# Kernel tuning notes

Measured on AMD Instinct MI355X. Metric: run time of the kernel, lower is better.

The kernel has to match this reference:

```python
import jax, jax.numpy as jnp
import numpy as np

B, T, E = 4, 2048, 256
H = 8
HD = E // H
FE = 4
L = 4
EPS = 1e-5


def _layernorm(x, g, b):
    mu = jnp.mean(x, axis=-1, keepdims=True)
    var = jnp.mean((x - mu) ** 2, axis=-1, keepdims=True)
    return (x - mu) * jax.lax.rsqrt(var + EPS) * g + b


def setup_inputs() -> dict:
    key = jax.random.key(0)
    ks = jax.random.split(key, 14)
    s = 0.02
    inp = {
        "x": jax.random.normal(ks[0], (B, T, E), dtype=jnp.float32),
        "qkv_w": jax.random.normal(ks[1], (L, E, 3 * E), dtype=jnp.float32) * s,
        "qkv_b": jnp.zeros((L, 3 * E), jnp.float32),
        "out_w": jax.random.normal(ks[2], (L, E, E), dtype=jnp.float32) * s,
        "out_b": jnp.zeros((L, E), jnp.float32),
        "ff1_w": jax.random.normal(ks[3], (L, E, FE * E), dtype=jnp.float32) * s,
        "ff1_b": jnp.zeros((L, FE * E), jnp.float32),
        "ff2_w": jax.random.normal(ks[4], (L, FE * E, E), dtype=jnp.float32) * s,
        "ff2_b": jnp.zeros((L, E), jnp.float32),
        "ln1_g": jnp.ones((L, E), jnp.float32),
        "ln1_b": jnp.zeros((L, E), jnp.float32),
        "ln2_g": jnp.ones((L, E), jnp.float32),
        "ln2_b": jnp.zeros((L, E), jnp.float32),
    }
    return inp


def _fourier_pe(x):
    # freqs over even indices: 10000^(-i/E), i = 0,2,...,E-2  -> E/2 freqs
    freqs = jnp.power(10000.0, -jnp.arange(0, E, 2, dtype=jnp.float32) / E)
    pos = jnp.arange(T, dtype=jnp.float32)[:, None]          # (T,1)
    sinusoid = pos * freqs[None, :]                            # (T, E/2)
    pe = jnp.concatenate([jnp.sin(sinusoid), jnp.cos(sinusoid)], axis=-1)  # (T,E)
    return x + pe[None, :, :]


def _forward(x, qkv_w, qkv_b, out_w, out_b, ff1_w, ff1_b, ff2_w, ff2_b,
             ln1_g, ln1_b, ln2_g, ln2_b):
    x = _fourier_pe(x)
    scale = 1.0 / np.sqrt(HD)
    for i in range(L):
        # attention (dropout = identity at eval)
        qkv = x @ qkv_w[i] + qkv_b[i]                          # (B,T,3E)
        qkv = qkv.reshape(B, T, H, 3, HD)                      # chunk of 3*hd -> (3,hd)
        q, k, v = qkv[..., 0, :], qkv[..., 1, :], qkv[..., 2, :]  # (B,T,H,HD)
        scores = jnp.einsum("bqhd,bkhd->bhqk", q, k) * scale   # (B,H,T,T)
        w = jax.nn.softmax(scores, axis=-1)
        attn = jnp.einsum("bhqk,bkhd->bqhd", w, v).reshape(B, T, E)
        attn = attn @ out_w[i] + out_b[i]
        x = _layernorm(x + attn, ln1_g[i], ln1_b[i])
        # feedforward
        h = jax.nn.relu(x @ ff1_w[i] + ff1_b[i])
        ff = h @ ff2_w[i] + ff2_b[i]
        x = _layernorm(x + ff, ln2_g[i], ln2_b[i])
    return x


def reference(x, qkv_w, qkv_b, out_w, out_b, ff1_w, ff1_b, ff2_w, ff2_b,
              ln1_g, ln1_b, ln2_g, ln2_b):
    return _forward(x, qkv_w, qkv_b, out_w, out_b, ff1_w, ff1_b, ff2_w, ff2_b,
                    ln1_g, ln1_b, ln2_g, ln2_b)
```

## Files before the change

kernel.cpp:

```cpp
#include <hip/hip_runtime.h>
#include <hip/hip_bf16.h>
#include <stdint.h>

typedef unsigned short u16;
typedef _Float16 f16;
typedef short vs8 __attribute__((ext_vector_type(8)));
typedef float vf4 __attribute__((ext_vector_type(4)));
typedef _Float16 vh2 __attribute__((ext_vector_type(2)));
typedef _Float16 vh4 __attribute__((ext_vector_type(4)));
typedef _Float16 vh8 __attribute__((ext_vector_type(8)));
typedef __fp16 hw2 __attribute__((ext_vector_type(2)));


__device__ __forceinline__ void gload16(const u16* g, u16* l) {
  __builtin_amdgcn_global_load_lds((const __attribute__((address_space(1))) void*)g,
                                   (__attribute__((address_space(3))) void*)l,
                                   16, 0, 0);
}

__device__ __forceinline__ float fexp2(float x) {
#if __has_builtin(__builtin_amdgcn_exp2f)
  return __builtin_amdgcn_exp2f(x);
#else
  return __expf(x * 0.69314718056f);
#endif
}

__global__ void pe_kernel(const float* __restrict__ x, __hip_bfloat16* __restrict__ Xb) {
  int row = blockIdx.x;
  int e = threadIdx.x;
  int t = row & 2047;
  int f = (e < 128) ? e : (e - 128);
  float freq = powf(10000.0f, -(float)f * (1.0f / 128.0f));
  float arg = (float)t * freq;
  float pe = (e < 128) ? sinf(arg) : cosf(arg);
  size_t idx = (size_t)row * 256 + e;
  Xb[idx] = __float2bfloat16(x[idx] + pe);
}

__global__ void transpose_cast(const float* __restrict__ in, u16* __restrict__ out,
                               int K, int N) {
  __shared__ float tile[32][33];
  int layer = blockIdx.z;
  int k0 = blockIdx.x * 32, n0 = blockIdx.y * 32;
  const float* ip = in + (size_t)layer * K * N;
  u16* op = out + (size_t)layer * N * K;
  int tx = threadIdx.x, ty = threadIdx.y;
#pragma unroll
  for (int r = 0; r < 4; ++r) {
    int k = ty + r * 8;
    tile[k][tx] = ip[(size_t)(k0 + k) * N + (n0 + tx)];
  }
  __syncthreads();
#pragma unroll
  for (int r = 0; r < 4; ++r) {
    int n = ty + r * 8;
    __hip_bfloat16 v = __float2bfloat16(tile[tx][n]);
    op[(size_t)(n0 + n) * K + (k0 + tx)] = *(u16*)&v;
  }
}

__global__ __launch_bounds__(256, 2) void gemm_relu(
    const u16* __restrict__ A, const u16* __restrict__ Bt,
    const float* __restrict__ bias, __hip_bfloat16* __restrict__ outB,
    int M, int N, int K) {
  __shared__ u16 As[128 * 32];
  __shared__ u16 Bs[128 * 32];
  int tid = threadIdx.x;
  int wave = tid >> 6, lane = tid & 63;
  int wm = wave & 1, wn = wave >> 1;
  int m0 = blockIdx.y * 128, n0 = blockIdx.x * 128;
  int lr = lane & 15, lq = lane >> 4;

  vf4 acc[4][4];
#pragma unroll
  for (int i = 0; i < 4; ++i)
#pragma unroll
    for (int j = 0; j < 4; ++j) {
      acc[i][j][0] = 0.f; acc[i][j][1] = 0.f; acc[i][j][2] = 0.f; acc[i][j][3] = 0.f;
    }

  int srow = wave * 16 + (lane >> 2);
  int scol = (lane & 3) * 8;
  const u16* ag = A + (size_t)(m0 + srow) * K + scol;
  const u16* bg = Bt + (size_t)(n0 + srow) * K + scol;
  u16* al = As + srow * 32 + scol;
  u16* bl = Bs + srow * 32 + scol;
  const size_t rstride = (size_t)64 * K;

  for (int k0 = 0; k0 < K; k0 += 32) {
    gload16(ag + k0, al);
    gload16(ag + k0 + rstride, al + 64 * 32);
    gload16(bg + k0, bl);
    gload16(bg + k0 + rstride, bl + 64 * 32);
    __syncthreads();
    vs8 av[4], bv[4];
#pragma unroll
    for (int i = 0; i < 4; ++i)
      av[i] = *(const vs8*)&As[(wm * 64 + i * 16 + lr) * 32 + lq * 8];
#pragma unroll
    for (int j = 0; j < 4; ++j)
      bv[j] = *(const vs8*)&Bs[(wn * 64 + j * 16 + lr) * 32 + lq * 8];
#pragma unroll
    for (int i = 0; i < 4; ++i)
#pragma unroll
      for (int j = 0; j < 4; ++j)
        acc[i][j] = __builtin_amdgcn_mfma_f32_16x16x32_bf16(av[i], bv[j], acc[i][j], 0, 0, 0);
    __syncthreads();
  }

#pragma unroll
  for (int i = 0; i < 4; ++i) {
    int row0 = m0 + wm * 64 + i * 16 + lq * 4;
#pragma unroll
    for (int j = 0; j < 4; ++j) {
      int col = n0 + wn * 64 + j * 16 + lr;
      float bb = bias[col];
#pragma unroll
      for (int r = 0; r < 4; ++r) {
        size_t idx = (size_t)(row0 + r) * N + col;
        outB[idx] = __float2bfloat16(fmaxf(acc[i][j][r] + bb, 0.0f));
      }
    }
  }
}

__global__ __launch_bounds__(256, 2) void gemm_qkv(
    const u16* __restrict__ A, const u16* __restrict__ Bt,
    const float* __restrict__ bias, f16* __restrict__ outH,
    int M, int N, int K) {
  __shared__ u16 As[64 * 32];
  __shared__ u16 Bs[128 * 32];
  int tid = threadIdx.x;
  int wave = tid >> 6, lane = tid & 63;
  int wm = wave & 1, wn = wave >> 1;
  int m0 = blockIdx.y * 64, n0 = blockIdx.x * 128;
  int lr = lane & 15, lq = lane >> 4;

  vf4 acc[2][4];
#pragma unroll
  for (int i = 0; i < 2; ++i)
#pragma unroll
    for (int j = 0; j < 4; ++j) { acc[i][j][0]=0.f; acc[i][j][1]=0.f; acc[i][j][2]=0.f; acc[i][j][3]=0.f; }

  int sr = tid >> 2, sc = (tid & 3) * 8;
  const u16* ag = A + (size_t)(m0 + sr) * K + sc;
  const u16* bg = Bt + (size_t)(n0 + sr) * K + sc;
  u16* al = As + sr * 32 + sc;
  u16* bl = Bs + sr * 32 + sc;

  for (int k0 = 0; k0 < K; k0 += 32) {
    gload16(ag + k0, al);
    gload16(bg + k0, bl);
    gload16(bg + k0 + (size_t)64 * K, bl + 64 * 32);
    __syncthreads();
    vs8 av[2], bv[4];
#pragma unroll
    for (int i = 0; i < 2; ++i)
      av[i] = *(const vs8*)&As[(wm * 32 + i * 16 + lr) * 32 + lq * 8];
#pragma unroll
    for (int j = 0; j < 4; ++j)
      bv[j] = *(const vs8*)&Bs[(wn * 64 + j * 16 + lr) * 32 + lq * 8];
#pragma unroll
    for (int i = 0; i < 2; ++i)
#pragma unroll
      for (int j = 0; j < 4; ++j)
        acc[i][j] = __builtin_amdgcn_mfma_f32_16x16x32_bf16(av[i], bv[j], acc[i][j], 0, 0, 0);
    __syncthreads();
  }

#pragma unroll
  for (int i = 0; i < 2; ++i) {
    int row0 = m0 + wm * 32 + i * 16 + lq * 4;
#pragma unroll
    for (int j = 0; j < 4; ++j) {
      int col = n0 + wn * 64 + j * 16 + lr;
      float bb = bias[col];
#pragma unroll
      for (int r = 0; r < 4; ++r)
        outH[(size_t)(row0 + r) * N + col] = (f16)(acc[i][j][r] + bb);
    }
  }
}

__global__ __launch_bounds__(512, 2) void gemm_ln(
    const u16* __restrict__ A, const u16* __restrict__ Bt,
    const float* __restrict__ bias, const __hip_bfloat16* __restrict__ res,
    const float* __restrict__ gam, const float* __restrict__ bet,
    __hip_bfloat16* __restrict__ outB, float* __restrict__ outF, int K) {
  __shared__ u16 As[32 * 32];
  __shared__ u16 Bs[256 * 32];
  __shared__ float ps[4][32], ps2[4][32], mur[32], rsr[32];
  int tid = threadIdx.x;
  int wave = tid >> 6, lane = tid & 63;
  int wm = wave & 1, wn = wave >> 1;
  int lr = lane & 15, lq = lane >> 4;
  int m0 = blockIdx.x * 32;

  vf4 acc[4];
#pragma unroll
  for (int j = 0; j < 4; ++j) { acc[j][0]=0.f; acc[j][1]=0.f; acc[j][2]=0.f; acc[j][3]=0.f; }

  int sr = tid >> 2, sc = (tid & 3) * 8;
  const u16* ag = A + (size_t)(m0 + sr) * K + sc;
  const u16* bg = Bt + (size_t)sr * K + sc;
  u16* al = As + sr * 32 + sc;
  u16* bl = Bs + sr * 32 + sc;

  for (int k0 = 0; k0 < K; k0 += 32) {
    if (tid < 128) gload16(ag + k0, al);
    gload16(bg + k0, bl);
    gload16(bg + k0 + (size_t)128 * K, bl + 128 * 32);
    __syncthreads();
    vs8 av, bv[4];
    av = *(const vs8*)&As[(wm * 16 + lr) * 32 + lq * 8];
#pragma unroll
    for (int j = 0; j < 4; ++j)
      bv[j] = *(const vs8*)&Bs[(wn * 64 + j * 16 + lr) * 32 + lq * 8];
#pragma unroll
    for (int j = 0; j < 4; ++j)
      acc[j] = __builtin_amdgcn_mfma_f32_16x16x32_bf16(av, bv[j], acc[j], 0, 0, 0);
    __syncthreads();
  }

  float sum_[4], sq_[4];
#pragma unroll
  for (int r = 0; r < 4; ++r) { sum_[r] = 0.f; sq_[r] = 0.f; }
#pragma unroll
  for (int j = 0; j < 4; ++j) {
    int col = wn * 64 + j * 16 + lr;
    float bb = bias[col];
#pragma unroll
    for (int r = 0; r < 4; ++r) {
      int row = m0 + wm * 16 + lq * 4 + r;
      float v = acc[j][r] + bb + __bfloat162float(res[(size_t)row * 256 + col]);
      acc[j][r] = v;
      sum_[r] += v;
      sq_[r] += v * v;
    }
  }
#pragma unroll
  for (int r = 0; r < 4; ++r) {
#pragma unroll
    for (int m = 1; m <= 8; m <<= 1) {
      sum_[r] += __shfl_xor(sum_[r], m);
      sq_[r]  += __shfl_xor(sq_[r], m);
    }
  }
  if (lr == 0) {
#pragma unroll
    for (int r = 0; r < 4; ++r) {
      int rl = wm * 16 + lq * 4 + r;
      ps[wn][rl] = sum_[r];
      ps2[wn][rl] = sq_[r];
    }
  }
  __syncthreads();
  if (tid < 32) {
    float s = ps[0][tid] + ps[1][tid] + ps[2][tid] + ps[3][tid];
    float s2 = ps2[0][tid] + ps2[1][tid] + ps2[2][tid] + ps2[3][tid];
    float mu = s * (1.0f / 256.0f);
    float var = s2 * (1.0f / 256.0f) - mu * mu;
    mur[tid] = mu;
    rsr[tid] = rsqrtf(var + 1e-5f);
  }
  __syncthreads();
#pragma unroll
  for (int r = 0; r < 4; ++r) {
    int rl = wm * 16 + lq * 4 + r;
    float mu = mur[rl], rs = rsr[rl];
    int row = m0 + rl;
#pragma unroll
    for (int j = 0; j < 4; ++j) {
      int col = wn * 64 + j * 16 + lr;
      float o = (acc[j][r] - mu) * rs * gam[col] + bet[col];
      size_t idx = (size_t)row * 256 + col;
      outB[idx] = __float2bfloat16(o);
      if (outF) outF[idx] = o;
    }
  }
}

__global__ __launch_bounds__(512, 4) void attn_mfma(const f16* __restrict__ qkv,
                                                    f16* __restrict__ Of,
                                                    float* __restrict__ lf) {
  __shared__ __align__(16) u16 lds[2][9344];
  int tid = threadIdx.x;
  int wave = tid >> 6, lane = tid & 63;
  int lr = lane & 15, quad = lane >> 4;

  int id = blockIdx.x;
  int xcd = id & 7, slot = id >> 3;
  int grp = xcd * 4 + (slot & 3);
  int qt = (slot >> 2) & 7;
  int split = slot >> 5;
  int b = grp >> 3, h = grp & 7;
  int q0 = qt * 256;
  int kv0 = split << 10;
  int rowbase = b * 2048;
  const f16* base_bh = qkv + (size_t)rowbase * 768 + h * 96;

  vh8 qf[2];
#pragma unroll
  for (int nt = 0; nt < 2; ++nt) {
    int qr = q0 + wave * 32 + nt * 16 + lr;
    vh8 t = *(const vh8*)(base_bh + (size_t)qr * 768 + quad * 8);
#pragma unroll
    for (int j = 0; j < 8; ++j) t[j] = t[j] * (f16)0.25508682f;
    qf[nt] = t;
  }

  vf4 O[2][2], lO[2];
#pragma unroll
  for (int a = 0; a < 2; ++a) {
    lO[a][0]=0.f; lO[a][1]=0.f; lO[a][2]=0.f; lO[a][3]=0.f;
#pragma unroll
    for (int d = 0; d < 2; ++d) { O[a][d][0]=0.f; O[a][d][1]=0.f; O[a][d][2]=0.f; O[a][d][3]=0.f; }
  }

  int srK = tid >> 2;
  int scK = (tid & 3) * 8;
  const f16* kg = base_bh + (size_t)(kv0 + srK) * 768 + 32 + scK;
  int kvp = tid >> 3;
  int d4 = (tid & 7) * 4;
  const f16* vg = base_bh + (size_t)(kv0 + kvp * 2) * 768 + 64 + d4;

  const vf4 z4 = {0.f, 0.f, 0.f, 0.f};
  const vh4 onesh = {(f16)1.0f, (f16)1.0f, (f16)1.0f, (f16)1.0f};
  const size_t cstep = (size_t)128 * 768;

  {
    vh8 k0 = *(const vh8*)kg;
    *(vh8*)&lds[0][srK * 40 + scK] = k0;
    vh4 a = *(const vh4*)vg;
    vh4 bb = *(const vh4*)(vg + 768);
    f16* vt0 = (f16*)&lds[0][5120];
#pragma unroll
    for (int i = 0; i < 4; ++i) {
      vh2 pr; pr[0] = a[i]; pr[1] = bb[i];
      *(vh2*)(vt0 + (d4 + i) * 132 + kvp * 2) = pr;
    }
  }
  __syncthreads();

  for (int c = 0; c < 8; ++c) {
    int cur = c & 1;
    const f16* Ks = (const f16*)&lds[cur][0];
    const f16* VT = (const f16*)&lds[cur][5120];

    vh8 kn; vh4 va, vb;
    if (c < 7) {
      kn = *(const vh8*)(kg + (size_t)(c + 1) * cstep);
      const f16* vp = vg + (size_t)(c + 1) * cstep;
      va = *(const vh4*)vp;
      vb = *(const vh4*)(vp + 768);
    }

#pragma unroll
    for (int t16 = 0; t16 < 8; ++t16) {
      vh8 ak = *(const vh8*)&Ks[(t16 * 16 + lr) * 40 + quad * 8];
      vf4 s0 = __builtin_amdgcn_mfma_f32_16x16x32_f16(ak, qf[0], z4, 0, 0, 0);
      vf4 s1 = __builtin_amdgcn_mfma_f32_16x16x32_f16(ak, qf[1], z4, 0, 0, 0);
      vh4 p0, p1;
      ((hw2*)&p0)[0] = __builtin_amdgcn_cvt_pkrtz(fexp2(s0[0]), fexp2(s0[1]));
      ((hw2*)&p0)[1] = __builtin_amdgcn_cvt_pkrtz(fexp2(s0[2]), fexp2(s0[3]));
      ((hw2*)&p1)[0] = __builtin_amdgcn_cvt_pkrtz(fexp2(s1[0]), fexp2(s1[1]));
      ((hw2*)&p1)[1] = __builtin_amdgcn_cvt_pkrtz(fexp2(s1[2]), fexp2(s1[3]));
      vh4 vf0 = *(const vh4*)&VT[(0 * 16 + lr) * 132 + t16 * 16 + quad * 4];
      vh4 vf1 = *(const vh4*)&VT[(1 * 16 + lr) * 132 + t16 * 16 + quad * 4];
      O[0][0] = __builtin_amdgcn_mfma_f32_16x16x16f16(p0, vf0, O[0][0], 0, 0, 0);
      O[0][1] = __builtin_amdgcn_mfma_f32_16x16x16f16(p0, vf1, O[0][1], 0, 0, 0);
      O[1][0] = __builtin_amdgcn_mfma_f32_16x16x16f16(p1, vf0, O[1][0], 0, 0, 0);
      O[1][1] = __builtin_amdgcn_mfma_f32_16x16x16f16(p1, vf1, O[1][1], 0, 0, 0);
      lO[0] = __builtin_amdgcn_mfma_f32_16x16x16f16(p0, onesh, lO[0], 0, 0, 0);
      lO[1] = __builtin_amdgcn_mfma_f32_16x16x16f16(p1, onesh, lO[1], 0, 0, 0);
    }

    if (c < 7) {
      *(vh8*)&lds[cur ^ 1][srK * 40 + scK] = kn;
      f16* vt1 = (f16*)&lds[cur ^ 1][5120];
#pragma unroll
      for (int i = 0; i < 4; ++i) {
        vh2 pr; pr[0] = va[i]; pr[1] = vb[i];
        *(vh2*)(vt1 + (d4 + i) * 132 + kvp * 2) = pr;
      }
    }
    __syncthreads();
  }

#pragma unroll
  for (int nt = 0; nt < 2; ++nt) {
#pragma unroll
    for (int r = 0; r < 4; ++r) {
      int tq = q0 + wave * 32 + nt * 16 + quad * 4 + r;
      if (lr == 0) lf[split * 65536 + grp * 2048 + tq] = lO[nt][r];
      int row = rowbase + tq;
#pragma unroll
      for (int dt = 0; dt < 2; ++dt) {
        int col = h * 32 + dt * 16 + lr;
        Of[(size_t)split * 2097152 + (size_t)row * 256 + col] = (f16)O[nt][dt][r];
      }
    }
  }
}

__global__ __launch_bounds__(256) void attn_combine(const f16* __restrict__ Of,
                                                    const float* __restrict__ lf,
                                                    __hip_bfloat16* __restrict__ out) {
  int idx = blockIdx.x * 256 + threadIdx.x;
  int row = idx >> 5;
  int col0 = (idx & 31) * 8;
  int grp = ((row >> 11) << 3) + (col0 >> 5);
  int t = row & 2047;
  float l = lf[grp * 2048 + t] + lf[65536 + grp * 2048 + t];
  float inv = 1.0f / l;
  size_t off = (size_t)row * 256 + col0;
  vh8 a = *(const vh8*)(Of + off);
  vh8 bq = *(const vh8*)(Of + 2097152 + off);
  union { vs8 v; u16 u[8]; } o;
#pragma unroll
  for (int j = 0; j < 8; ++j) {
    __hip_bfloat16 hb = __float2bfloat16(((float)a[j] + (float)bq[j]) * inv);
    o.u[j] = *(u16*)&hb;
  }
  *(vs8*)((u16*)out + off) = o.v;
}

extern "C" void kernel_launch(void* const* d_in, const int* in_sizes, int n_in,
                              void* d_out, int out_size, void* d_ws, size_t ws_size,
                              hipStream_t stream) {
  (void)in_sizes; (void)n_in; (void)out_size; (void)ws_size;
  const float* x     = (const float*)d_in[0];
  const float* qkv_b = (const float*)d_in[2];
  const float* out_b = (const float*)d_in[4];
  const float* ff1_b = (const float*)d_in[6];
  const float* ff2_b = (const float*)d_in[8];
  const float* ln1_g = (const float*)d_in[9];
  const float* ln1_b = (const float*)d_in[10];
  const float* ln2_g = (const float*)d_in[11];
  const float* ln2_b = (const float*)d_in[12];

  char* ws = (char*)d_ws;
  f16*            Of    = (f16*)(ws + 0);
  __hip_bfloat16* Xb    = (__hip_bfloat16*)(ws + 8388608);
  float*          lf    = (float*)(ws + 12582912);
  __hip_bfloat16* attnB = (__hip_bfloat16*)(ws + 20971520);
  f16*            qkvH  = (f16*)(ws + 25165824);
  __hip_bfloat16* hB    = (__hip_bfloat16*)(ws + 20971520);
  u16* qkvwT = (u16*)(ws + 37748736);
  u16* outwT = (u16*)(ws + 39321600);
  u16* ff1wT = (u16*)(ws + 39845888);
  u16* ff2wT = (u16*)(ws + 41943040);

  pe_kernel<<<8192, 256, 0, stream>>>(x, Xb);
  transpose_cast<<<dim3(8, 24, 4), dim3(32, 8), 0, stream>>>((const float*)d_in[1], qkvwT, 256, 768);
  transpose_cast<<<dim3(8, 8, 4),  dim3(32, 8), 0, stream>>>((const float*)d_in[3], outwT, 256, 256);
  transpose_cast<<<dim3(8, 32, 4), dim3(32, 8), 0, stream>>>((const float*)d_in[5], ff1wT, 256, 1024);
  transpose_cast<<<dim3(32, 8, 4), dim3(32, 8), 0, stream>>>((const float*)d_in[7], ff2wT, 1024, 256);

  for (int l = 0; l < 4; ++l) {
    gemm_qkv<<<dim3(6, 128), 256, 0, stream>>>((const u16*)Xb, qkvwT + (size_t)l * 768 * 256,
        qkv_b + l * 768, qkvH, 8192, 768, 256);
    attn_mfma<<<512, 512, 0, stream>>>(qkvH, Of, lf);
    attn_combine<<<1024, 256, 0, stream>>>(Of, lf, attnB);
    gemm_ln<<<256, 512, 0, stream>>>((const u16*)attnB, outwT + (size_t)l * 256 * 256,
        out_b + l * 256, Xb, ln1_g + l * 256, ln1_b + l * 256, Xb, nullptr, 256);
    gemm_relu<<<dim3(8, 64), 256, 0, stream>>>((const u16*)Xb, ff1wT + (size_t)l * 1024 * 256,
        ff1_b + l * 1024, hB, 8192, 1024, 256);
    float* lnout = (l == 3) ? (float*)d_out : nullptr;
    gemm_ln<<<256, 512, 0, stream>>>((const u16*)hB, ff2wT + (size_t)l * 256 * 1024,
        ff2_b + l * 256, Xb, ln2_g + l * 256, ln2_b + l * 256, Xb, lnout, 1024);
  }
}
```

Baseline: 463.4 us.

## Fuse attention combine into out-proj GEMM, enlarge QKV tile, merge prep kernels

Removes the attn_combine kernel by having the output-projection GEMM read both split-K partial outputs and normalize them by the summed softmax denominators while staging A into LDS. The QKV GEMM tile grows from 64 to 128 rows. The four weight transpose launches are merged into one, and the positional-encoding kernel is vectorized using hardware sin/cos on a range-reduced argument. The fused A path uses regular loads plus conversion instead of async global-to-LDS loads, which may slow the GEMM's main loop, and the bigger QKV tile halves the number of blocks.

```diff
diff --git a/kernel.cpp b/kernel.cpp
--- a/kernel.cpp
+++ b/kernel.cpp
@@ -27,34 +27,56 @@
 }
 
 __global__ void pe_kernel(const float* __restrict__ x, __hip_bfloat16* __restrict__ Xb) {
-  int row = blockIdx.x;
-  int e = threadIdx.x;
+  int gid = blockIdx.x * 256 + threadIdx.x;
+  int row = gid >> 6;
+  int e0 = (gid & 63) * 4;
   int t = row & 2047;
-  int f = (e < 128) ? e : (e - 128);
-  float freq = powf(10000.0f, -(float)f * (1.0f / 128.0f));
-  float arg = (float)t * freq;
-  float pe = (e < 128) ? sinf(arg) : cosf(arg);
-  size_t idx = (size_t)row * 256 + e;
-  Xb[idx] = __float2bfloat16(x[idx] + pe);
-}
-
-__global__ void transpose_cast(const float* __restrict__ in, u16* __restrict__ out,
-                               int K, int N) {
+  int f0 = (e0 < 128) ? e0 : (e0 - 128);
+  const float c = -13.287712379549449f / 128.0f;
+  const float inv2pi = 0.15915494309189535f;
+  float4 xv = *(const float4*)(x + (size_t)row * 256 + e0);
+  union { vs8 v; u16 u[8]; } dummy; (void)dummy;
+  u16 o[4];
+#pragma unroll
+  for (int j = 0; j < 4; ++j) {
+    float freq = fexp2(c * (float)(f0 + j));
+    float rev = (float)t * freq * inv2pi;
+    rev = rev - floorf(rev);
+    float pe = (e0 < 128) ? __builtin_amdgcn_sinf(rev) : __builtin_amdgcn_cosf(rev);
+    float xin = (j == 0) ? xv.x : (j == 1) ? xv.y : (j == 2) ? xv.z : xv.w;
+    __hip_bfloat16 hb = __float2bfloat16(xin + pe);
+    o[j] = *(u16*)&hb;
+  }
+  *(uint2*)((u16*)Xb + (size_t)row * 256 + e0) = *(uint2*)o;
+}
+
+__global__ void transpose_cast_all(
+    const float* __restrict__ w0, const float* __restrict__ w1,
+    const float* __restrict__ w2, const float* __restrict__ w3,
+    u16* __restrict__ o0, u16* __restrict__ o1,
+    u16* __restrict__ o2, u16* __restrict__ o3) {
   __shared__ float tile[32][33];
-  int layer = blockIdx.z;
-  int k0 = blockIdx.x * 32, n0 = blockIdx.y * 32;
-  const float* ip = in + (size_t)layer * K * N;
-  u16* op = out + (size_t)layer * N * K;
+  int flat = blockIdx.x;
+  int layer = flat / 768;
+  int r = flat - layer * 768;
+  const float* ip; u16* op; int K, N, kt, nt;
+  if (r < 192)      {              ip = w0; op = o0; K = 256;  N = 768;  kt = r & 7;  nt = r >> 3; }
+  else if (r < 256) { int q=r-192; ip = w1; op = o1; K = 256;  N = 256;  kt = q & 7;  nt = q >> 3; }
+  else if (r < 512) { int q=r-256; ip = w2; op = o2; K = 256;  N = 1024; kt = q & 7;  nt = q >> 3; }
+  else              { int q=r-512; ip = w3; op = o3; K = 1024; N = 256;  kt = q & 31; nt = q >> 5; }
+  ip += (size_t)layer * K * N;
+  op += (size_t)layer * N * K;
+  int k0 = kt * 32, n0 = nt * 32;
   int tx = threadIdx.x, ty = threadIdx.y;
 #pragma unroll
-  for (int r = 0; r < 4; ++r) {
-    int k = ty + r * 8;
+  for (int rr = 0; rr < 4; ++rr) {
+    int k = ty + rr * 8;
     tile[k][tx] = ip[(size_t)(k0 + k) * N + (n0 + tx)];
   }
   __syncthreads();
 #pragma unroll
-  for (int r = 0; r < 4; ++r) {
-    int n = ty + r * 8;
+  for (int rr = 0; rr < 4; ++rr) {
+    int n = ty + rr * 8;
     __hip_bfloat16 v = __float2bfloat16(tile[tx][n]);
     op[(size_t)(n0 + n) * K + (k0 + tx)] = *(u16*)&v;
   }
@@ -125,44 +147,49 @@
   }
 }
 
-__global__ __launch_bounds__(256, 2) void gemm_qkv(
+__global__ __launch_bounds__(256, 2) void gemm_qkv128(
     const u16* __restrict__ A, const u16* __restrict__ Bt,
     const float* __restrict__ bias, f16* __restrict__ outH,
     int M, int N, int K) {
-  __shared__ u16 As[64 * 32];
+  __shared__ u16 As[128 * 32];
   __shared__ u16 Bs[128 * 32];
   int tid = threadIdx.x;
   int wave = tid >> 6, lane = tid & 63;
   int wm = wave & 1, wn = wave >> 1;
-  int m0 = blockIdx.y * 64, n0 = blockIdx.x * 128;
+  int m0 = blockIdx.y * 128, n0 = blockIdx.x * 128;
   int lr = lane & 15, lq = lane >> 4;
 
-  vf4 acc[2][4];
-#pragma unroll
-  for (int i = 0; i < 2; ++i)
-#pragma unroll
-    for (int j = 0; j < 4; ++j) { acc[i][j][0]=0.f; acc[i][j][1]=0.f; acc[i][j][2]=0.f; acc[i][j][3]=0.f; }
-
-  int sr = tid >> 2, sc = (tid & 3) * 8;
-  const u16* ag = A + (size_t)(m0 + sr) * K + sc;
-  const u16* bg = Bt + (size_t)(n0 + sr) * K + sc;
-  u16* al = As + sr * 32 + sc;
-  u16* bl = Bs + sr * 32 + sc;
+  vf4 acc[4][4];
+#pragma unroll
+  for (int i = 0; i < 4; ++i)
+#pragma unroll
+    for (int j = 0; j < 4; ++j) {
+      acc[i][j][0] = 0.f; acc[i][j][1] = 0.f; acc[i][j][2] = 0.f; acc[i][j][3] = 0.f;
+    }
+
+  int srow = wave * 16 + (lane >> 2);
+  int scol = (lane & 3) * 8;
+  const u16* ag = A + (size_t)(m0 + srow) * K + scol;
+  const u16* bg = Bt + (size_t)(n0 + srow) * K + scol;
+  u16* al = As + srow * 32 + scol;
+  u16* bl = Bs + srow * 32 + scol;
+  const size_t rstride = (size_t)64 * K;
 
   for (int k0 = 0; k0 < K; k0 += 32) {
     gload16(ag + k0, al);
+    gload16(ag + k0 + rstride, al + 64 * 32);
     gload16(bg + k0, bl);
-    gload16(bg + k0 + (size_t)64 * K, bl + 64 * 32);
-    __syncthreads();
-    vs8 av[2], bv[4];
-#pragma unroll
-    for (int i = 0; i < 2; ++i)
-      av[i] = *(const vs8*)&As[(wm * 32 + i * 16 + lr) * 32 + lq * 8];
+    gload16(bg + k0 + rstride, bl + 64 * 32);
+    __syncthreads();
+    vs8 av[4], bv[4];
+#pragma unroll
+    for (int i = 0; i < 4; ++i)
+      av[i] = *(const vs8*)&As[(wm * 64 + i * 16 + lr) * 32 + lq * 8];
 #pragma unroll
     for (int j = 0; j < 4; ++j)
       bv[j] = *(const vs8*)&Bs[(wn * 64 + j * 16 + lr) * 32 + lq * 8];
 #pragma unroll
-    for (int i = 0; i < 2; ++i)
+    for (int i = 0; i < 4; ++i)
 #pragma unroll
       for (int j = 0; j < 4; ++j)
         acc[i][j] = __builtin_amdgcn_mfma_f32_16x16x32_bf16(av[i], bv[j], acc[i][j], 0, 0, 0);
@@ -170,8 +197,8 @@
   }
 
 #pragma unroll
-  for (int i = 0; i < 2; ++i) {
-    int row0 = m0 + wm * 32 + i * 16 + lq * 4;
+  for (int i = 0; i < 4; ++i) {
+    int row0 = m0 + wm * 64 + i * 16 + lq * 4;
 #pragma unroll
     for (int j = 0; j < 4; ++j) {
       int col = n0 + wn * 64 + j * 16 + lr;
@@ -187,10 +214,12 @@
     const u16* __restrict__ A, const u16* __restrict__ Bt,
     const float* __restrict__ bias, const __hip_bfloat16* __restrict__ res,
     const float* __restrict__ gam, const float* __restrict__ bet,
-    __hip_bfloat16* __restrict__ outB, float* __restrict__ outF, int K) {
+    __hip_bfloat16* __restrict__ outB, float* __restrict__ outF, int K,
+    const f16* __restrict__ OfA, const float* __restrict__ lf) {
   __shared__ u16 As[32 * 32];
   __shared__ u16 Bs[256 * 32];
   __shared__ float ps[4][32], ps2[4][32], mur[32], rsr[32];
+  __shared__ float invs[8][32];
   int tid = threadIdx.x;
   int wave = tid >> 6, lane = tid & 63;
   int wm = wave & 1, wn = wave >> 1;
@@ -207,8 +236,34 @@
   u16* al = As + sr * 32 + sc;
   u16* bl = Bs + sr * 32 + sc;
 
+  if (OfA) {
+    if (tid < 256) {
+      int h = tid >> 5, rl = tid & 31;
+      int row = m0 + rl, bb_ = row >> 11, t = row & 2047;
+      int g = bb_ * 8 + h;
+      invs[h][rl] = 1.0f / (lf[g * 2048 + t] + lf[65536 + g * 2048 + t]);
+    }
+    __syncthreads();
+  }
+
   for (int k0 = 0; k0 < K; k0 += 32) {
-    if (tid < 128) gload16(ag + k0, al);
+    if (tid < 128) {
+      if (OfA) {
+        size_t off = (size_t)(m0 + sr) * 256 + k0 + sc;
+        vh8 a0 = *(const vh8*)(OfA + off);
+        vh8 a1 = *(const vh8*)(OfA + 2097152 + off);
+        float inv = invs[k0 >> 5][sr];
+        union { vs8 v; u16 u[8]; } pk;
+#pragma unroll
+        for (int j = 0; j < 8; ++j) {
+          __hip_bfloat16 hb = __float2bfloat16(((float)a0[j] + (float)a1[j]) * inv);
+          pk.u[j] = *(u16*)&hb;
+        }
+        *(vs8*)al = pk.v;
+      } else {
+        gload16(ag + k0, al);
+      }
+    }
     gload16(bg + k0, bl);
     gload16(bg + k0 + (size_t)128 * K, bl + 128 * 32);
     __syncthreads();
@@ -404,28 +459,6 @@
   }
 }
 
-__global__ __launch_bounds__(256) void attn_combine(const f16* __restrict__ Of,
-                                                    const float* __restrict__ lf,
-                                                    __hip_bfloat16* __restrict__ out) {
-  int idx = blockIdx.x * 256 + threadIdx.x;
-  int row = idx >> 5;
-  int col0 = (idx & 31) * 8;
-  int grp = ((row >> 11) << 3) + (col0 >> 5);
-  int t = row & 2047;
-  float l = lf[grp * 2048 + t] + lf[65536 + grp * 2048 + t];
-  float inv = 1.0f / l;
-  size_t off = (size_t)row * 256 + col0;
-  vh8 a = *(const vh8*)(Of + off);
-  vh8 bq = *(const vh8*)(Of + 2097152 + off);
-  union { vs8 v; u16 u[8]; } o;
-#pragma unroll
-  for (int j = 0; j < 8; ++j) {
-    __hip_bfloat16 hb = __float2bfloat16(((float)a[j] + (float)bq[j]) * inv);
-    o.u[j] = *(u16*)&hb;
-  }
-  *(vs8*)((u16*)out + off) = o.v;
-}
-
 extern "C" void kernel_launch(void* const* d_in, const int* in_sizes, int n_in,
                               void* d_out, int out_size, void* d_ws, size_t ws_size,
                               hipStream_t stream) {
@@ -444,7 +477,6 @@
   f16*            Of    = (f16*)(ws + 0);
   __hip_bfloat16* Xb    = (__hip_bfloat16*)(ws + 8388608);
   float*          lf    = (float*)(ws + 12582912);
-  __hip_bfloat16* attnB = (__hip_bfloat16*)(ws + 20971520);
   f16*            qkvH  = (f16*)(ws + 25165824);
   __hip_bfloat16* hB    = (__hip_bfloat16*)(ws + 20971520);
   u16* qkvwT = (u16*)(ws + 37748736);
@@ -452,23 +484,21 @@
   u16* ff1wT = (u16*)(ws + 39845888);
   u16* ff2wT = (u16*)(ws + 41943040);
 
-  pe_kernel<<<8192, 256, 0, stream>>>(x, Xb);
-  transpose_cast<<<dim3(8, 24, 4), dim3(32, 8), 0, stream>>>((const float*)d_in[1], qkvwT, 256, 768);
-  transpose_cast<<<dim3(8, 8, 4),  dim3(32, 8), 0, stream>>>((const float*)d_in[3], outwT, 256, 256);
-  transpose_cast<<<dim3(8, 32, 4), dim3(32, 8), 0, stream>>>((const float*)d_in[5], ff1wT, 256, 1024);
-  transpose_cast<<<dim3(32, 8, 4), dim3(32, 8), 0, stream>>>((const float*)d_in[7], ff2wT, 1024, 256);
+  pe_kernel<<<2048, 256, 0, stream>>>(x, Xb);
+  transpose_cast_all<<<3072, dim3(32, 8), 0, stream>>>(
+      (const float*)d_in[1], (const float*)d_in[3], (const float*)d_in[5], (const float*)d_in[7],
+      qkvwT, outwT, ff1wT, ff2wT);
 
   for (int l = 0; l < 4; ++l) {
-    gemm_qkv<<<dim3(6, 128), 256, 0, stream>>>((const u16*)Xb, qkvwT + (size_t)l * 768 * 256,
+    gemm_qkv128<<<dim3(6, 64), 256, 0, stream>>>((const u16*)Xb, qkvwT + (size_t)l * 768 * 256,
         qkv_b + l * 768, qkvH, 8192, 768, 256);
     attn_mfma<<<512, 512, 0, stream>>>(qkvH, Of, lf);
-    attn_combine<<<1024, 256, 0, stream>>>(Of, lf, attnB);
-    gemm_ln<<<256, 512, 0, stream>>>((const u16*)attnB, outwT + (size_t)l * 256 * 256,
-        out_b + l * 256, Xb, ln1_g + l * 256, ln1_b + l * 256, Xb, nullptr, 256);
+    gemm_ln<<<256, 512, 0, stream>>>(nullptr, outwT + (size_t)l * 256 * 256,
+        out_b + l * 256, Xb, ln1_g + l * 256, ln1_b + l * 256, Xb, nullptr, 256, Of, lf);
     gemm_relu<<<dim3(8, 64), 256, 0, stream>>>((const u16*)Xb, ff1wT + (size_t)l * 1024 * 256,
         ff1_b + l * 1024, hB, 8192, 1024, 256);
     float* lnout = (l == 3) ? (float*)d_out : nullptr;
     gemm_ln<<<256, 512, 0, stream>>>((const u16*)hB, ff2wT + (size_t)l * 256 * 1024,
-        ff2_b + l * 256, Xb, ln2_g + l * 256, ln2_b + l * 256, Xb, lnout, 1024);
-  }
-}
+        ff2_b + l * 256, Xb, ln2_g + l * 256, ln2_b + l * 256, Xb, lnout, 1024, nullptr, nullptr);
+  }
+}
```

After: 443.7 us. -4.3%, faster.
